# Performance work log

Hardware: AMD Instinct MI355X
Metric: run time of the kernel (lower is better)

Reference implementation:

```python
import jax, jax.numpy as jnp
import numpy as np


def setup_inputs() -> dict:
    key = jax.random.key(0)
    ks = jax.random.split(key, 12)
    B, N, Dv, E, H, V, T = 128, 196, 512, 512, 1024, 10000, 20
    s = 0.02  # small init scale for numerical stability
    f = lambda k, shp: (jax.random.normal(k, shp, jnp.float32) * s)
    return {
        "features": jax.random.normal(ks[0], (B, N, Dv), jnp.float32),
        "captions": jax.random.randint(ks[1], (B, T), 0, V),
        "W_init_h": f(ks[2], (H, Dv)),
        "W_init_c": f(ks[3], (H, Dv)),
        "W_attn_v": f(ks[4], (1, Dv)),
        "b_attn_v": jnp.zeros((1,), jnp.float32),
        "W_attn_h": f(ks[5], (1, H)),
        "b_attn_h": jnp.zeros((1,), jnp.float32),
        "embed_table": f(ks[6], (V, E)),
        "W_ih": f(ks[7], (4 * H, Dv + E)),
        "W_hh": f(ks[8], (4 * H, H)),
        "b_ih": jnp.zeros((4 * H,), jnp.float32),
        "b_hh": jnp.zeros((4 * H,), jnp.float32),
        "W_out": f(ks[9], (V, H)),
        "b_out": jnp.zeros((V,), jnp.float32),
    }


def reference(features, captions, W_init_h, W_init_c, W_attn_v, b_attn_v,
              W_attn_h, b_attn_h, embed_table, W_ih, W_hh, b_ih, b_hh,
              W_out, b_out):
    B, N, Dv = features.shape
    # _init_hidden: mean over vis_num of linear projections (division by vis_num)
    h0 = jnp.sum(jnp.einsum('bnd,hd->bnh', features, W_init_h), axis=1) / N
    c0 = jnp.sum(jnp.einsum('bnd,hd->bnh', features, W_init_c), axis=1) / N

    emb = embed_table[captions]                      # B,T,E
    emb_t_major = jnp.swapaxes(emb, 0, 1)            # T,B,E
    # visual attention logits are time-invariant; precompute once
    att_v = jnp.einsum('bnd,od->bno', features, W_attn_v) + b_attn_v  # B,N,1

    def step(carry, emb_t):
        h, c = carry
        # soft attention over vis_num locations
        att_h = (h @ W_attn_h.T + b_attn_h)[:, None, :]   # B,1,1
        alpha = jax.nn.softmax(att_v + att_h, axis=1)     # B,N,1
        ctx = jnp.sum(features * alpha, axis=1)           # B,Dv
        # single-step LSTM (PyTorch gate order: i, f, g, o)
        x = jnp.concatenate([ctx, emb_t], axis=-1)        # B,Dv+E
        gates = x @ W_ih.T + h @ W_hh.T + b_ih + b_hh     # B,4H
        i, fg, g, o = jnp.split(gates, 4, axis=-1)
        c_new = jax.nn.sigmoid(fg) * c + jax.nn.sigmoid(i) * jnp.tanh(g)
        h_new = jax.nn.sigmoid(o) * jnp.tanh(c_new)
        words = h_new @ W_out.T + b_out                   # B,V
        return (h_new, c_new), words

    _, word_space = jax.lax.scan(step, (h0, c0), emb_t_major)  # T,B,V
    # pack_padded_sequence with all-equal lengths flattens time-major -> (T*B, V)
    packed = word_space.reshape(-1, word_space.shape[-1])
    return jax.nn.log_softmax(packed, axis=1), jax.nn.softmax(packed, axis=1)
```

## Files before the change

### kernel.cpp

```cpp
#include <hip/hip_runtime.h>
#include <math.h>

#define B    128
#define NLOC 196
#define DV   512
#define EMB  512
#define HD   1024
#define VV   10000
#define TT   20
#define G4   4096
#define VPAD 10112
#define BH   (B*HD)

typedef short bf16x8 __attribute__((ext_vector_type(8)));
typedef short s16x4  __attribute__((ext_vector_type(4)));
typedef float f32x4  __attribute__((ext_vector_type(4)));

__device__ __forceinline__ unsigned short f2bf(float x) {
    unsigned u = __builtin_bit_cast(unsigned, x);
    unsigned r = (u + 0x7fffu + ((u >> 16) & 1u)) >> 16;
    return (unsigned short)r;
}
__device__ __forceinline__ float bf2f(short s) {
    unsigned u = ((unsigned)(unsigned short)s) << 16;
    return __builtin_bit_cast(float, u);
}

__device__ __forceinline__ void gload_lds16(const void* g, void* lds) {
    __builtin_amdgcn_global_load_lds(
        (const __attribute__((address_space(1))) void*)g,
        (__attribute__((address_space(3))) void*)lds, 16, 0, 0);
}


__global__ void attv_kernel(const float* __restrict__ feat, const float* __restrict__ wv,
                            const float* __restrict__ bv, float* __restrict__ attv) {
    int row  = blockIdx.x;
    int lane = threadIdx.x;
    const float* p = feat + (size_t)row * DV;
    float s = 0.f;
    for (int k = lane; k < DV; k += 64) s += p[k] * wv[k];
    for (int off = 32; off > 0; off >>= 1) s += __shfl_down(s, off);
    if (lane == 0) attv[row] = s + bv[0];
}

__global__ void alpha_kernel(const float* __restrict__ attv, float* __restrict__ alpha) {
    int b   = blockIdx.x;
    int tid = threadIdx.x;
    __shared__ float red[256];
    float v = (tid < NLOC) ? attv[b * NLOC + tid] : -1e30f;
    red[tid] = v; __syncthreads();
    for (int s = 128; s > 0; s >>= 1) { if (tid < s) red[tid] = fmaxf(red[tid], red[tid + s]); __syncthreads(); }
    float m = red[0]; __syncthreads();
    float e = (tid < NLOC) ? expf(v - m) : 0.f;
    red[tid] = e; __syncthreads();
    for (int s = 128; s > 0; s >>= 1) { if (tid < s) red[tid] += red[tid + s]; __syncthreads(); }
    float sum = red[0];
    if (tid < NLOC) alpha[b * NLOC + tid] = e / sum;
}

__global__ void fmeanctx_kernel(const float* __restrict__ feat, const float* __restrict__ alpha,
                                short* __restrict__ fmean_b, short* __restrict__ ctx_b) {
    int idx = blockIdx.x * blockDim.x + threadIdx.x;
    if (idx >= B * DV) return;
    int b = idx / DV, d = idx % DV;
    const float* p = feat + (size_t)b * NLOC * DV + d;
    const float* a = alpha + b * NLOC;
    float sm = 0.f, sc = 0.f;
    for (int n = 0; n < NLOC; ++n) {
        float v = p[(size_t)n * DV];
        sm += v;
        sc += a[n] * v;
    }
    fmean_b[idx] = (short)f2bf(sm * (1.0f / NLOC));
    ctx_b[idx]   = (short)f2bf(sc);
}

__global__ void emb_gather_kernel(const int* __restrict__ captions, const float* __restrict__ table,
                                  short* __restrict__ emb_b) {
    size_t q = (size_t)blockIdx.x * blockDim.x + threadIdx.x;
    if (q >= (size_t)TT * B * EMB / 4) return;
    size_t idx = q * 4;
    int k = (int)(idx % EMB);
    int r = (int)(idx / EMB);
    int t = r / B, b = r % B;
    int cap = captions[b * TT + t];
    float4 v = *(const float4*)&table[(size_t)cap * EMB + k];
    s16x4 o = { (short)f2bf(v.x), (short)f2bf(v.y), (short)f2bf(v.z), (short)f2bf(v.w) };
    *(s16x4*)&emb_b[idx] = o;
}

__global__ void c0cvt_kernel(const short* __restrict__ hc_b, float* __restrict__ cbuf) {
    int idx = blockIdx.x * blockDim.x + threadIdx.x;
    if (idx >= B * HD) return;
    cbuf[idx] = bf2f(hc_b[(size_t)(idx >> 10) * 2048 + 1024 + (idx & 1023)]);
}

#define N_WOUT ((size_t)VPAD * HD / 4)
#define N_WIH  ((size_t)G4 * HD / 4)
#define N_WHH  ((size_t)G4 * HD / 4)
#define N_WINI ((size_t)HD * DV / 4)
__global__ void convert_all_kernel(const float* __restrict__ W_out, short* __restrict__ Wout_b,
                                   const float* __restrict__ W_ih,  short* __restrict__ Wih_b,
                                   const float* __restrict__ W_hh,  short* __restrict__ Whh_b,
                                   const float* __restrict__ W_ini_h, short* __restrict__ Wini_h_b,
                                   const float* __restrict__ W_ini_c, short* __restrict__ Wini_c_b) {
    size_t q = (size_t)blockIdx.x * blockDim.x + threadIdx.x;
    size_t idx;
    if (q < N_WOUT) {
        idx = q * 4;
        size_t n = (size_t)VV * HD;
        s16x4 o = {0, 0, 0, 0};
        if (idx < n) {
            float4 v = *(const float4*)&W_out[idx];
            o = s16x4{ (short)f2bf(v.x), (short)f2bf(v.y), (short)f2bf(v.z), (short)f2bf(v.w) };
        }
        *(s16x4*)&Wout_b[idx] = o;
        return;
    }
    q -= N_WOUT;
    if (q < N_WIH) {
        idx = q * 4;
        float4 v = *(const float4*)&W_ih[idx];
        s16x4 o = { (short)f2bf(v.x), (short)f2bf(v.y), (short)f2bf(v.z), (short)f2bf(v.w) };
        *(s16x4*)&Wih_b[idx] = o;
        return;
    }
    q -= N_WIH;
    if (q < N_WHH) {
        idx = q * 4;
        int k = (int)(idx & (HD - 1));
        int P = (int)(idx >> 10);
        int u = P >> 2, g = P & 3;
        float4 v = *(const float4*)&W_hh[(size_t)(g * HD + u) * HD + k];
        s16x4 o = { (short)f2bf(v.x), (short)f2bf(v.y), (short)f2bf(v.z), (short)f2bf(v.w) };
        *(s16x4*)&Whh_b[idx] = o;
        return;
    }
    q -= N_WHH;
    if (q < N_WINI) {
        idx = q * 4;
        float4 v = *(const float4*)&W_ini_h[idx];
        s16x4 o = { (short)f2bf(v.x), (short)f2bf(v.y), (short)f2bf(v.z), (short)f2bf(v.w) };
        *(s16x4*)&Wini_h_b[idx] = o;
        return;
    }
    q -= N_WINI;
    if (q < N_WINI) {
        idx = q * 4;
        float4 v = *(const float4*)&W_ini_c[idx];
        s16x4 o = { (short)f2bf(v.x), (short)f2bf(v.y), (short)f2bf(v.z), (short)f2bf(v.w) };
        *(s16x4*)&Wini_c_b[idx] = o;
    }
}

template<int BN, int WR, int WC, bool BF16OUT>
__global__ __launch_bounds__(256)
void gemm_bf16(const short* __restrict__ A, const short* __restrict__ Bw,
               void* __restrict__ C,
               const float* __restrict__ bias0, const float* __restrict__ bias1,
               int NY, int M, int N, int K, int lda, int ldb, int ldc) {
    constexpr int BM = 128;
    constexpr int BK = 32;
    constexpr int WM = BM / WR;
    constexpr int WN = BN / WC;
    constexpr int FM = WM / 16;
    constexpr int FN = WN / 16;
    __shared__ __align__(16) short As[BM * BK];
    __shared__ __align__(16) short Bs[BN * BK];
    const int tid  = threadIdx.x;
    const int wave = tid >> 6, lane = tid & 63;
    const int wr = wave / WC, wc = wave % WC;

    const int nwg = gridDim.x;
    const int qq = nwg >> 3, rr8 = nwg & 7;
    const int p = blockIdx.x;
    const int xcd = p & 7, slot = p >> 3;
    const int lwg = (xcd < rr8) ? (xcd * (qq + 1) + slot)
                                : (rr8 * (qq + 1) + (xcd - rr8) * qq + slot);
    const int m0 = (lwg % NY) * BM;
    const int n0 = (lwg / NY) * BN;
    const int laneoff = lane * 16;

    f32x4 acc[FM][FN] = {};

    for (int k0 = 0; k0 < K; k0 += BK) {
        #pragma unroll
        for (int r = 0; r < 2; ++r) {
            int o   = r * 4096 + wave * 1024 + laneoff;
            int row = o >> 6;
            int gr  = (o >> 4) & 3;
            int col = ((gr ^ ((row >> 1) & 3)) << 3);
            gload_lds16(A + (size_t)(m0 + row) * lda + k0 + col,
                        (char*)As + r * 4096 + wave * 1024);
        }
        constexpr int BBYTES = BN * BK * 2;
        if constexpr (BBYTES >= 4096) {
            #pragma unroll
            for (int r = 0; r < BBYTES / 4096; ++r) {
                int o   = r * 4096 + wave * 1024 + laneoff;
                int row = o >> 6;
                int gr  = (o >> 4) & 3;
                int col = ((gr ^ ((row >> 1) & 3)) << 3);
                gload_lds16(Bw + (size_t)(n0 + row) * ldb + k0 + col,
                            (char*)Bs + r * 4096 + wave * 1024);
            }
        } else {
            constexpr int NW = BBYTES / 1024;
            if (wave < NW) {
                int o   = wave * 1024 + laneoff;
                int row = o >> 6;
                int gr  = (o >> 4) & 3;
                int col = ((gr ^ ((row >> 1) & 3)) << 3);
                gload_lds16(Bw + (size_t)(n0 + row) * ldb + k0 + col,
                            (char*)Bs + wave * 1024);
            }
        }
        __syncthreads();

        bf16x8 a[FM], b[FN];
        const int kfrg = lane >> 4;
        #pragma unroll
        for (int i = 0; i < FM; ++i) {
            int row = wr * WM + i * 16 + (lane & 15);
            a[i] = *(const bf16x8*)&As[row * BK + ((kfrg ^ ((row >> 1) & 3)) << 3)];
        }
        #pragma unroll
        for (int j = 0; j < FN; ++j) {
            int row = wc * WN + j * 16 + (lane & 15);
            b[j] = *(const bf16x8*)&Bs[row * BK + ((kfrg ^ ((row >> 1) & 3)) << 3)];
        }
        #pragma unroll
        for (int i = 0; i < FM; ++i)
            #pragma unroll
            for (int j = 0; j < FN; ++j)
                acc[i][j] = __builtin_amdgcn_mfma_f32_16x16x32_bf16(a[i], b[j], acc[i][j], 0, 0, 0);
        __syncthreads();
    }

    #pragma unroll
    for (int i = 0; i < FM; ++i) {
        #pragma unroll
        for (int j = 0; j < FN; ++j) {
            int col = n0 + wc * WN + j * 16 + (lane & 15);
            if (col >= N) continue;
            float bv = (bias0 ? bias0[col] : 0.f) + (bias1 ? bias1[col] : 0.f);
            #pragma unroll
            for (int q = 0; q < 4; ++q) {
                int row = m0 + wr * WM + i * 16 + (lane >> 4) * 4 + q;
                if (row < M) {
                    float v = acc[i][j][q] + bv;
                    if constexpr (BF16OUT)
                        ((short*)C)[(size_t)row * ldc + col] = (short)f2bf(v);
                    else
                        ((float*)C)[(size_t)row * ldc + col] = v;
                }
            }
        }
    }
}

__global__ __launch_bounds__(256)
void gemm_k64(const short* __restrict__ A, const short* __restrict__ Bw,
              short* __restrict__ C,
              const float* __restrict__ bias0, const short* __restrict__ addrow,
              int NY, int M, int N, int K, int lda, int ldb, int ldc) {
    __shared__ __align__(16) short As[128 * 64];
    __shared__ __align__(16) short Bs[128 * 64];
    const int tid  = threadIdx.x;
    const int wave = tid >> 6, lane = tid & 63;
    const int wr = wave >> 1, wc = wave & 1;

    const int nwg = gridDim.x;
    const int qq = nwg >> 3, rr8 = nwg & 7;
    const int p = blockIdx.x;
    const int xcd = p & 7, slot = p >> 3;
    const int lwg = (xcd < rr8) ? (xcd * (qq + 1) + slot)
                                : (rr8 * (qq + 1) + (xcd - rr8) * qq + slot);
    const int m0 = (lwg % NY) * 128;
    const int n0 = (lwg / NY) * 128;
    const int laneoff = lane * 16;
    const int kfrg = lane >> 4;

    f32x4 acc[4][4] = {};

    for (int k0 = 0; k0 < K; k0 += 64) {
        #pragma unroll
        for (int r = 0; r < 4; ++r) {
            int o   = r * 4096 + wave * 1024 + laneoff;
            int row = o >> 7;
            int gr  = (o >> 4) & 7;
            int col = ((gr ^ (row & 7)) << 3);
            gload_lds16(A + (size_t)(m0 + row) * lda + k0 + col,
                        (char*)As + r * 4096 + wave * 1024);
            gload_lds16(Bw + (size_t)(n0 + row) * ldb + k0 + col,
                        (char*)Bs + r * 4096 + wave * 1024);
        }
        __syncthreads();

        #pragma unroll
        for (int kh = 0; kh < 2; ++kh) {
            bf16x8 a[4], b[4];
            #pragma unroll
            for (int i = 0; i < 4; ++i) {
                int row = wr * 64 + i * 16 + (lane & 15);
                a[i] = *(const bf16x8*)&As[row * 64 + (((kh * 4 + kfrg) ^ (row & 7)) << 3)];
            }
            #pragma unroll
            for (int j = 0; j < 4; ++j) {
                int row = wc * 64 + j * 16 + (lane & 15);
                b[j] = *(const bf16x8*)&Bs[row * 64 + (((kh * 4 + kfrg) ^ (row & 7)) << 3)];
            }
            #pragma unroll
            for (int i = 0; i < 4; ++i)
                #pragma unroll
                for (int j = 0; j < 4; ++j)
                    acc[i][j] = __builtin_amdgcn_mfma_f32_16x16x32_bf16(a[i], b[j], acc[i][j], 0, 0, 0);
        }
        __syncthreads();
    }

    #pragma unroll
    for (int i = 0; i < 4; ++i) {
        #pragma unroll
        for (int j = 0; j < 4; ++j) {
            int col = n0 + wc * 64 + j * 16 + (lane & 15);
            if (col >= N) continue;
            float bv = bias0 ? bias0[col] : 0.f;
            #pragma unroll
            for (int q = 0; q < 4; ++q) {
                int row = m0 + wr * 64 + i * 16 + (lane >> 4) * 4 + q;
                if (row < M) {
                    float v = acc[i][j][q] + bv;
                    if (addrow) v += bf2f(addrow[(size_t)(row & 127) * ldc + col]);
                    C[(size_t)row * ldc + col] = (short)f2bf(v);
                }
            }
        }
    }
}

__global__ __launch_bounds__(256)
void lstm_step9(const short* __restrict__ Hprev, int lda, const short* __restrict__ Whh_p,
                const short* __restrict__ pre_t,
                float* __restrict__ cbuf, short* __restrict__ Hall_t) {
    __shared__ __align__(16) short As[32 * 512];
    __shared__ __align__(16) short Ws[32 * 512];
    __shared__ float gsm[4][32][8];
    const int tid  = threadIdx.x;
    const int lane = tid & 63, wave = tid >> 6;
    const int n0 = blockIdx.x * 32;
    const int m0 = blockIdx.y * 32;

    const int mi = wave >> 1, ni = wave & 1;
    const int arowL = mi * 16 + (lane & 15);
    const int browL = ni * 16 + (lane & 15);
    const int kg    = lane >> 4;

    f32x4 acc = {};

    for (int h2 = 0; h2 < 2; ++h2) {
        const int k0 = h2 * 512;
        #pragma unroll
        for (int it = 0; it < 8; ++it) {
            int fg  = it * 256 + tid;
            int row = fg >> 6;
            int g   = fg & 63;
            int col = (g ^ (row & 7)) * 8;
            gload_lds16(Hprev + (size_t)(m0 + row) * lda + k0 + col,
                        (char*)As + it * 4096 + wave * 1024);
            gload_lds16(Whh_p + (size_t)(n0 + row) * HD + k0 + col,
                        (char*)Ws + it * 4096 + wave * 1024);
        }
        __syncthreads();
        #pragma unroll
        for (int ks = 0; ks < 16; ++ks) {
            int lg = ks * 4 + kg;
            bf16x8 a = *(const bf16x8*)((const char*)As + arowL * 1024 + ((lg ^ (arowL & 7)) << 4));
            bf16x8 w = *(const bf16x8*)((const char*)Ws + browL * 1024 + ((lg ^ (browL & 7)) << 4));
            acc = __builtin_amdgcn_mfma_f32_16x16x32_bf16(a, w, acc, 0, 0, 0);
        }
        __syncthreads();
    }

    #pragma unroll
    for (int q = 0; q < 4; ++q) {
        int rr = mi * 16 + (lane >> 4) * 4 + q;
        gsm[browL & 3][rr][browL >> 2] = acc[q];
    }
    __syncthreads();

    const int m = tid >> 3, u8 = tid & 7;
    const int r = m0 + m, u = blockIdx.x * 8 + u8;
    size_t pb = (size_t)r * G4 + u;
    float gi  = gsm[0][m][u8] + bf2f(pre_t[pb]);
    float gf  = gsm[1][m][u8] + bf2f(pre_t[pb + HD]);
    float gg2 = gsm[2][m][u8] + bf2f(pre_t[pb + 2 * HD]);
    float go  = gsm[3][m][u8] + bf2f(pre_t[pb + 3 * HD]);
    float si = 1.f / (1.f + expf(-gi));
    float sf = 1.f / (1.f + expf(-gf));
    float so = 1.f / (1.f + expf(-go));
    float cn = sf * cbuf[(size_t)r * HD + u] + si * tanhf(gg2);
    float hn = so * tanhf(cn);
    cbuf[(size_t)r * HD + u] = cn;
    Hall_t[(size_t)r * HD + u] = (short)f2bf(hn);
}

__global__ __launch_bounds__(512)
void softmax_kernel(const short* __restrict__ wbf, float* __restrict__ logout,
                    float* __restrict__ smout) {
    __shared__ float rowbuf[VV];
    __shared__ float red[512];
    int r = blockIdx.x;
    int tid = threadIdx.x;
    const short* row = wbf + (size_t)r * VV;
    float m = -1e30f;
    for (int i = tid; i < VV; i += 512) {
        float v = bf2f(row[i]);
        rowbuf[i] = v;
        m = fmaxf(m, v);
    }
    red[tid] = m; __syncthreads();
    for (int s = 256; s > 0; s >>= 1) { if (tid < s) red[tid] = fmaxf(red[tid], red[tid + s]); __syncthreads(); }
    m = red[0]; __syncthreads();
    float sum = 0.f;
    for (int i = tid; i < VV; i += 512) sum += expf(rowbuf[i] - m);
    red[tid] = sum; __syncthreads();
    for (int s = 256; s > 0; s >>= 1) { if (tid < s) red[tid] += red[tid + s]; __syncthreads(); }
    sum = red[0];
    float inv = 1.f / sum;
    float lz = logf(sum);
    for (int i = tid; i < VV; i += 512) {
        float x = rowbuf[i];
        smout[(size_t)r * VV + i]  = expf(x - m) * inv;
        logout[(size_t)r * VV + i] = x - m - lz;
    }
}

extern "C" void kernel_launch(void* const* d_in, const int* in_sizes, int n_in,
                              void* d_out, int out_size, void* d_ws, size_t ws_size,
                              hipStream_t stream) {
    const float* features    = (const float*)d_in[0];
    const int*   captions    = (const int*)  d_in[1];
    const float* W_init_h    = (const float*)d_in[2];
    const float* W_init_c    = (const float*)d_in[3];
    const float* W_attn_v    = (const float*)d_in[4];
    const float* b_attn_v    = (const float*)d_in[5];
    const float* embed_table = (const float*)d_in[8];
    const float* W_ih        = (const float*)d_in[9];
    const float* W_hh        = (const float*)d_in[10];
    const float* b_ih        = (const float*)d_in[11];
    const float* b_hh        = (const float*)d_in[12];
    const float* W_out       = (const float*)d_in[13];
    const float* b_out       = (const float*)d_in[14];

    float* out   = (float*)d_out;
    float* words = out;
    float* s2    = out + (size_t)TT * B * VV;

    short* gate_pre_b = (short*)s2;
    short* Hall_b   = (short*)(s2 + (size_t)10485760);
    short* Wout_b   = (short*)(s2 + (size_t)10485760 + 1310720);
    short* Wih_b    = Wout_b + (size_t)VPAD * HD;
    short* Whh_b    = Wih_b  + (size_t)G4 * HD;
    short* Wini_h_b = Whh_b  + (size_t)G4 * HD;
    short* Wini_c_b = Wini_h_b + (size_t)HD * DV;

    char* w = (char*)d_ws;
    size_t off = 0;
    auto alloc = [&](size_t bytes) { void* p = w + off; off = (off + bytes + 255) & ~255UL; return p; };
    float* attv   = (float*)alloc((size_t)B * NLOC * 4);
    float* alpha  = (float*)alloc((size_t)B * NLOC * 4);
    short* gctx_b = (short*)alloc((size_t)B * G4 * 2);
    float* cbuf   = (float*)alloc((size_t)B * HD * 4);
    short* fmean_b= (short*)alloc((size_t)B * DV * 2);
    short* ctx_b  = (short*)alloc((size_t)B * DV * 2);
    short* hc_b   = (short*)alloc((size_t)B * 2048 * 2);
    short* emb_b  = (short*)alloc((size_t)TT * B * EMB * 2);
    short* words_bf = (short*)alloc((size_t)TT * B * VV * 2);

    {
        size_t total = N_WOUT + N_WIH + N_WHH + 2 * N_WINI;
        convert_all_kernel<<<(total + 255) / 256, 256, 0, stream>>>(
            W_out, Wout_b, W_ih, Wih_b, W_hh, Whh_b,
            W_init_h, Wini_h_b, W_init_c, Wini_c_b);
    }

    attv_kernel<<<B * NLOC, 64, 0, stream>>>(features, W_attn_v, b_attn_v, attv);
    alpha_kernel<<<B, 256, 0, stream>>>(attv, alpha);
    fmeanctx_kernel<<<(B * DV + 255) / 256, 256, 0, stream>>>(features, alpha, fmean_b, ctx_b);
    emb_gather_kernel<<<((size_t)TT * B * EMB / 4 + 255) / 256, 256, 0, stream>>>(
        captions, embed_table, emb_b);

    gemm_bf16<32, 4, 1, true><<<dim3(2048 / 32), 256, 0, stream>>>(
        fmean_b, Wini_h_b, hc_b, nullptr, nullptr, 1, B, 2048, DV, DV, DV, 2048);
    c0cvt_kernel<<<(B * HD + 255) / 256, 256, 0, stream>>>(hc_b, cbuf);

    gemm_bf16<32, 4, 1, true><<<dim3(G4 / 32), 256, 0, stream>>>(
        ctx_b, Wih_b, gctx_b, b_ih, b_hh, 1, B, G4, DV, DV, HD, G4);
    gemm_k64<<<dim3((G4 / 128) * (TT * B / 128)), 256, 0, stream>>>(
        emb_b, Wih_b + DV, gate_pre_b, nullptr, gctx_b, TT * B / 128,
        TT * B, G4, EMB, EMB, DV + EMB, G4);

    for (int t = 0; t < TT; ++t) {
        const short* Hprev = (t == 0) ? hc_b : (Hall_b + (size_t)(t - 1) * BH);
        int lda = (t == 0) ? 2048 : HD;
        lstm_step9<<<dim3(G4 / 32, B / 32), 256, 0, stream>>>(
            Hprev, lda, Whh_b, gate_pre_b + (size_t)t * B * G4,
            cbuf, Hall_b + (size_t)t * BH);
    }

    gemm_k64<<<dim3((VPAD / 128) * (TT * B / 128)), 256, 0, stream>>>(
        Hall_b, Wout_b, words_bf, b_out, nullptr, TT * B / 128,
        TT * B, VV, HD, HD, HD, VV);
    softmax_kernel<<<TT * B, 512, 0, stream>>>(words_bf, words, s2);
}
```

Measured before the change: 426.3 us.

## Overlap per-step output projection with next LSTM step in one launch

Merges the LSTM recurrent step and the vocabulary projection of the previous timestep's hidden state into a single kernel launch. Blocks with y>0 compute the gate GEMM and cell update, while y=0 blocks compute words for step t-1. The final step's projection is done by a small gemm launch. The aim is to use idle CUs during the latency-bound recurrent steps instead of running one large output GEMM afterward. In exchange, shared memory per block grows to 68KB, which may reduce occupancy for the LSTM blocks, and the slow word blocks may lengthen each step.

```diff
diff --git a/kernel.cpp b/kernel.cpp
--- a/kernel.cpp
+++ b/kernel.cpp
@@ -341,69 +341,135 @@
 }
 
 __global__ __launch_bounds__(256)
-void lstm_step9(const short* __restrict__ Hprev, int lda, const short* __restrict__ Whh_p,
-                const short* __restrict__ pre_t,
-                float* __restrict__ cbuf, short* __restrict__ Hall_t) {
-    __shared__ __align__(16) short As[32 * 512];
-    __shared__ __align__(16) short Ws[32 * 512];
-    __shared__ float gsm[4][32][8];
+void step_words(const short* __restrict__ Hprev, int lda, const short* __restrict__ Whh_p,
+                const short* __restrict__ pre_t, float* __restrict__ cbuf,
+                short* __restrict__ Hall_t,
+                const short* __restrict__ Wout_b, short* __restrict__ Cw,
+                const float* __restrict__ b_out, int doWords) {
+    __shared__ __align__(16) char smem[69632];
     const int tid  = threadIdx.x;
     const int lane = tid & 63, wave = tid >> 6;
-    const int n0 = blockIdx.x * 32;
-    const int m0 = blockIdx.y * 32;
-
-    const int mi = wave >> 1, ni = wave & 1;
-    const int arowL = mi * 16 + (lane & 15);
-    const int browL = ni * 16 + (lane & 15);
-    const int kg    = lane >> 4;
-
-    f32x4 acc = {};
-
-    for (int h2 = 0; h2 < 2; ++h2) {
-        const int k0 = h2 * 512;
-        #pragma unroll
-        for (int it = 0; it < 8; ++it) {
-            int fg  = it * 256 + tid;
-            int row = fg >> 6;
-            int g   = fg & 63;
-            int col = (g ^ (row & 7)) * 8;
-            gload_lds16(Hprev + (size_t)(m0 + row) * lda + k0 + col,
-                        (char*)As + it * 4096 + wave * 1024);
-            gload_lds16(Whh_p + (size_t)(n0 + row) * HD + k0 + col,
-                        (char*)Ws + it * 4096 + wave * 1024);
+
+    if (blockIdx.y > 0) {
+        short* As = (short*)smem;
+        short* Ws = (short*)(smem + 32768);
+        float* gsmf = (float*)(smem + 65536);
+        const int n0 = blockIdx.x * 32;
+        const int m0 = (blockIdx.y - 1) * 32;
+
+        const int mi = wave >> 1, ni = wave & 1;
+        const int arowL = mi * 16 + (lane & 15);
+        const int browL = ni * 16 + (lane & 15);
+        const int kg    = lane >> 4;
+
+        f32x4 acc = {};
+
+        for (int h2 = 0; h2 < 2; ++h2) {
+            const int k0 = h2 * 512;
+            #pragma unroll
+            for (int it = 0; it < 8; ++it) {
+                int fg  = it * 256 + tid;
+                int row = fg >> 6;
+                int g   = fg & 63;
+                int col = (g ^ (row & 7)) * 8;
+                gload_lds16(Hprev + (size_t)(m0 + row) * lda + k0 + col,
+                            (char*)As + it * 4096 + wave * 1024);
+                gload_lds16(Whh_p + (size_t)(n0 + row) * HD + k0 + col,
+                            (char*)Ws + it * 4096 + wave * 1024);
+            }
+            __syncthreads();
+            #pragma unroll
+            for (int ks = 0; ks < 16; ++ks) {
+                int lg = ks * 4 + kg;
+                bf16x8 a = *(const bf16x8*)((const char*)As + arowL * 1024 + ((lg ^ (arowL & 7)) << 4));
+                bf16x8 w = *(const bf16x8*)((const char*)Ws + browL * 1024 + ((lg ^ (browL & 7)) << 4));
+                acc = __builtin_amdgcn_mfma_f32_16x16x32_bf16(a, w, acc, 0, 0, 0);
+            }
+            __syncthreads();
+        }
+
+        #pragma unroll
+        for (int q = 0; q < 4; ++q) {
+            int rr = mi * 16 + (lane >> 4) * 4 + q;
+            gsmf[((browL & 3) * 32 + rr) * 8 + (browL >> 2)] = acc[q];
         }
         __syncthreads();
-        #pragma unroll
-        for (int ks = 0; ks < 16; ++ks) {
-            int lg = ks * 4 + kg;
-            bf16x8 a = *(const bf16x8*)((const char*)As + arowL * 1024 + ((lg ^ (arowL & 7)) << 4));
-            bf16x8 w = *(const bf16x8*)((const char*)Ws + browL * 1024 + ((lg ^ (browL & 7)) << 4));
-            acc = __builtin_amdgcn_mfma_f32_16x16x32_bf16(a, w, acc, 0, 0, 0);
-        }
-        __syncthreads();
-    }
-
-    #pragma unroll
-    for (int q = 0; q < 4; ++q) {
-        int rr = mi * 16 + (lane >> 4) * 4 + q;
-        gsm[browL & 3][rr][browL >> 2] = acc[q];
-    }
-    __syncthreads();
-
-    const int m = tid >> 3, u8 = tid & 7;
-    const int r = m0 + m, u = blockIdx.x * 8 + u8;
-    size_t pb = (size_t)r * G4 + u;
-    float gi  = gsm[0][m][u8] + bf2f(pre_t[pb]);
-    float gf  = gsm[1][m][u8] + bf2f(pre_t[pb + HD]);
-    float gg2 = gsm[2][m][u8] + bf2f(pre_t[pb + 2 * HD]);
-    float go  = gsm[3][m][u8] + bf2f(pre_t[pb + 3 * HD]);
-    float si = 1.f / (1.f + expf(-gi));
-    float sf = 1.f / (1.f + expf(-gf));
-    float so = 1.f / (1.f + expf(-go));
-    float cn = sf * cbuf[(size_t)r * HD + u] + si * tanhf(gg2);
-    float hn = so * tanhf(cn);
-    cbuf[(size_t)r * HD + u] = cn;
-    Hall_t[(size_t)r * HD + u] = (short)f2bf(hn);
+
+        const int m = tid >> 3, u8 = tid & 7;
+        const int r = m0 + m, u = blockIdx.x * 8 + u8;
+        size_t pb = (size_t)r * G4 + u;
+        float gi  = gsmf[(0 * 32 + m) * 8 + u8] + bf2f(pre_t[pb]);
+        float gf  = gsmf[(1 * 32 + m) * 8 + u8] + bf2f(pre_t[pb + HD]);
+        float gg2 = gsmf[(2 * 32 + m) * 8 + u8] + bf2f(pre_t[pb + 2 * HD]);
+        float go  = gsmf[(3 * 32 + m) * 8 + u8] + bf2f(pre_t[pb + 3 * HD]);
+        float si = 1.f / (1.f + expf(-gi));
+        float sf = 1.f / (1.f + expf(-gf));
+        float so = 1.f / (1.f + expf(-go));
+        float cn = sf * cbuf[(size_t)r * HD + u] + si * tanhf(gg2);
+        float hn = so * tanhf(cn);
+        cbuf[(size_t)r * HD + u] = cn;
+        Hall_t[(size_t)r * HD + u] = (short)f2bf(hn);
+    } else {
+        if (!doWords || blockIdx.x >= VPAD / 128) return;
+        short* Aw  = (short*)smem;
+        short* Bs2 = (short*)(smem + 16384);
+        const int n0 = blockIdx.x * 128;
+        const int wr = wave >> 1, wc = wave & 1;
+        const int laneoff = lane * 16;
+        const int kfrg = lane >> 4;
+
+        f32x4 acc[4][4] = {};
+
+        for (int k0 = 0; k0 < HD; k0 += 64) {
+            #pragma unroll
+            for (int r = 0; r < 4; ++r) {
+                int o   = r * 4096 + wave * 1024 + laneoff;
+                int row = o >> 7;
+                int gr  = (o >> 4) & 7;
+                int col = ((gr ^ (row & 7)) << 3);
+                gload_lds16(Hprev + (size_t)row * HD + k0 + col,
+                            (char*)Aw + r * 4096 + wave * 1024);
+                gload_lds16(Wout_b + (size_t)(n0 + row) * HD + k0 + col,
+                            (char*)Bs2 + r * 4096 + wave * 1024);
+            }
+            __syncthreads();
+            #pragma unroll
+            for (int kh = 0; kh < 2; ++kh) {
+                bf16x8 a[4], b[4];
+                #pragma unroll
+                for (int i = 0; i < 4; ++i) {
+                    int row = wr * 64 + i * 16 + (lane & 15);
+                    a[i] = *(const bf16x8*)&Aw[row * 64 + (((kh * 4 + kfrg) ^ (row & 7)) << 3)];
+                }
+                #pragma unroll
+                for (int j = 0; j < 4; ++j) {
+                    int row = wc * 64 + j * 16 + (lane & 15);
+                    b[j] = *(const bf16x8*)&Bs2[row * 64 + (((kh * 4 + kfrg) ^ (row & 7)) << 3)];
+                }
+                #pragma unroll
+                for (int i = 0; i < 4; ++i)
+                    #pragma unroll
+                    for (int j = 0; j < 4; ++j)
+                        acc[i][j] = __builtin_amdgcn_mfma_f32_16x16x32_bf16(a[i], b[j], acc[i][j], 0, 0, 0);
+            }
+            __syncthreads();
+        }
+
+        #pragma unroll
+        for (int i = 0; i < 4; ++i) {
+            #pragma unroll
+            for (int j = 0; j < 4; ++j) {
+                int col = n0 + wc * 64 + j * 16 + (lane & 15);
+                if (col >= VV) continue;
+                float bv = b_out[col];
+                #pragma unroll
+                for (int q = 0; q < 4; ++q) {
+                    int row = wr * 64 + i * 16 + (lane >> 4) * 4 + q;
+                    Cw[(size_t)row * VV + col] = (short)f2bf(acc[i][j][q] + bv);
+                }
+            }
+        }
+    }
 }
 
 __global__ __launch_bounds__(512)
@@ -505,13 +571,15 @@
     for (int t = 0; t < TT; ++t) {
         const short* Hprev = (t == 0) ? hc_b : (Hall_b + (size_t)(t - 1) * BH);
         int lda = (t == 0) ? 2048 : HD;
-        lstm_step9<<<dim3(G4 / 32, B / 32), 256, 0, stream>>>(
-            Hprev, lda, Whh_b, gate_pre_b + (size_t)t * B * G4,
-            cbuf, Hall_b + (size_t)t * BH);
-    }
-
-    gemm_k64<<<dim3((VPAD / 128) * (TT * B / 128)), 256, 0, stream>>>(
-        Hall_b, Wout_b, words_bf, b_out, nullptr, TT * B / 128,
-        TT * B, VV, HD, HD, HD, VV);
+        short* Cw = (t == 0) ? words_bf : (words_bf + (size_t)(t - 1) * B * VV);
+        step_words<<<dim3(128, 5), 256, 0, stream>>>(
+            Hprev, lda, Whh_b, gate_pre_b + (size_t)t * B * G4, cbuf,
+            Hall_b + (size_t)t * BH, Wout_b, Cw, b_out, t > 0 ? 1 : 0);
+    }
+
+    gemm_k64<<<dim3(VPAD / 128), 256, 0, stream>>>(
+        Hall_b + (size_t)(TT - 1) * BH, Wout_b,
+        words_bf + (size_t)(TT - 1) * B * VV, b_out, nullptr,
+        1, B, VV, HD, HD, HD, VV);
     softmax_kernel<<<TT * B, 512, 0, stream>>>(words_bf, words, s2);
 }
```

New measurement: 673.2 us. +57.9%, slower.
